# Kernel tuning notes

Measured on AMD Instinct MI355X. Metric: run time of the kernel, lower is better.

## Reference

```python
import jax, jax.numpy as jnp
import numpy as np

B, K, C, H, W = 32, 4, 256, 32, 32
MID = 32  # ceil((C//8)/8)*8
EPS = 1e-5


def setup_inputs() -> dict:
    key = jax.random.key(0)
    ks = jax.random.split(key, 8)
    scale1 = 1.0 / np.sqrt((K + 1) * C)
    scale2 = 1.0 / np.sqrt(MID)
    return {
        "y": jax.random.normal(ks[0], (B, C, H, W), jnp.float32),
        "x0": jax.random.normal(ks[1], (B, C, H, W), jnp.float32),
        "x1": jax.random.normal(ks[2], (B, C, H, W), jnp.float32),
        "x2": jax.random.normal(ks[3], (B, C, H, W), jnp.float32),
        "x3": jax.random.normal(ks[4], (B, C, H, W), jnp.float32),
        "conv1_w": jax.random.normal(ks[5], (MID, (K + 1) * C), jnp.float32) * scale1,
        "bn_gamma": jnp.ones((MID,), jnp.float32),
        "bn_beta": jnp.zeros((MID,), jnp.float32),
        "bn_mean": jnp.zeros((MID,), jnp.float32),
        "bn_var": jnp.ones((MID,), jnp.float32),
        "conv2_w": jax.random.normal(ks[6], ((K + 1) * C, MID), jnp.float32) * scale2,
        "conv2_b": jnp.zeros(((K + 1) * C,), jnp.float32),
    }


def reference(y, x0, x1, x2, x3, conv1_w, bn_gamma, bn_beta, bn_mean, bn_var, conv2_w, conv2_b):
    # Stack K branch feature maps: [B, K, C, H, W]
    xs = jnp.stack([x0, x1, x2, x3], axis=1)
    # Global-average-pooled gate features (1x1 spatial -> plain vectors)
    m_y = jnp.mean(y, axis=(2, 3))            # [B, C]
    m_x = jnp.mean(xs, axis=(3, 4))           # [B, K, C]
    feats = jnp.concatenate([m_y[:, None, :], m_x], axis=1).reshape(B, (K + 1) * C)
    # 1x1 conv -> BN (inference) -> ReLU -> 1x1 conv (all on 1x1 spatial = GEMM)
    h = feats @ conv1_w.T                      # [B, MID]
    h = (h - bn_mean) * (bn_gamma / jnp.sqrt(bn_var + EPS)) + bn_beta
    h = jax.nn.relu(h)
    w = (h @ conv2_w.T + conv2_b).reshape(B, K + 1, C)
    w1 = jax.nn.sigmoid(w[:, 0])               # [B, C] self gate
    w2 = jax.nn.softmax(w[:, 1:], axis=1)      # [B, K, C] branch gates (softmax over K)
    # Gated weighted sum of branches (GatedFunction.forward)
    z = jnp.einsum('bkc,bkchw->bchw', w2, xs)
    return y * w1[:, :, None, None] + z
```

## Files before the change

### kernel.cpp

```cpp
#include <hip/hip_runtime.h>
#include <math.h>

#define B 32
#define K 4
#define C 256
#define HW 1024
#define NT 5
#define MID 32
#define FEAT 1280
#define EPS 1e-5f

__global__ __launch_bounds__(256) void mean_kernel(
    const float* __restrict__ y,
    const float* __restrict__ x0, const float* __restrict__ x1,
    const float* __restrict__ x2, const float* __restrict__ x3,
    float* __restrict__ feats)
{
    const int wave = (blockIdx.x << 2) + (threadIdx.x >> 6);
    const int lane = threadIdx.x & 63;
    const int t    = wave >> 11;
    const int rem  = wave & 2047;
    const int b    = rem >> 6;
    const int g    = rem & 63;
    const float* src = (t == 0) ? y : (t == 1) ? x0 : (t == 2) ? x1
                                    : (t == 3) ? x2 : x3;
    const float4* p = (const float4*)(src + ((size_t)(b * C) + g * 4) * HW);

    float4 v[4][4];
#pragma unroll
    for (int s = 0; s < 4; ++s)
#pragma unroll
        for (int j = 0; j < 4; ++j)
            v[s][j] = p[s * 256 + j * 64 + lane];

    float s0 = 0.f, s1 = 0.f, s2 = 0.f, s3 = 0.f;
#pragma unroll
    for (int j = 0; j < 4; ++j) {
        s0 += v[0][j].x + v[0][j].y + v[0][j].z + v[0][j].w;
        s1 += v[1][j].x + v[1][j].y + v[1][j].z + v[1][j].w;
        s2 += v[2][j].x + v[2][j].y + v[2][j].z + v[2][j].w;
        s3 += v[3][j].x + v[3][j].y + v[3][j].z + v[3][j].w;
    }
#pragma unroll
    for (int m = 32; m >= 1; m >>= 1) {
        s0 += __shfl_xor(s0, m);
        s1 += __shfl_xor(s1, m);
        s2 += __shfl_xor(s2, m);
        s3 += __shfl_xor(s3, m);
    }
    if (lane == 0) {
        float4 r = make_float4(s0, s1, s2, s3);
        r.x *= (1.0f / 1024.0f); r.y *= (1.0f / 1024.0f);
        r.z *= (1.0f / 1024.0f); r.w *= (1.0f / 1024.0f);
        *((float4*)&feats[b * FEAT + t * C + g * 4]) = r;
    }
}

__global__ __launch_bounds__(512) void gate_kernel(
    const float* __restrict__ feats,
    const float* __restrict__ conv1_w,
    const float* __restrict__ bn_gamma, const float* __restrict__ bn_beta,
    const float* __restrict__ bn_mean,  const float* __restrict__ bn_var,
    const float* __restrict__ conv2_w,
    const float* __restrict__ conv2_b,
    float* __restrict__ gates)
{
    __shared__ __align__(16) float feats_s[FEAT];
    __shared__ float h_s[MID];

    const int b    = blockIdx.x;
    const int tid  = threadIdx.x;
    const int wave = tid >> 6;
    const int lane = tid & 63;

    for (int i = tid; i < FEAT; i += 512) feats_s[i] = feats[b * FEAT + i];
    __syncthreads();

    const float4* fs = (const float4*)feats_s;
    float4 wv[4][5];
#pragma unroll
    for (int r = 0; r < 4; ++r) {
        const float4* wp = (const float4*)(conv1_w + (wave * 4 + r) * FEAT);
#pragma unroll
        for (int k = 0; k < 5; ++k) wv[r][k] = wp[lane + 64 * k];
    }
    float a0 = 0.f, a1 = 0.f, a2 = 0.f, a3 = 0.f;
#pragma unroll
    for (int k = 0; k < 5; ++k) {
        float4 f = fs[lane + 64 * k];
        a0 += wv[0][k].x * f.x + wv[0][k].y * f.y + wv[0][k].z * f.z + wv[0][k].w * f.w;
        a1 += wv[1][k].x * f.x + wv[1][k].y * f.y + wv[1][k].z * f.z + wv[1][k].w * f.w;
        a2 += wv[2][k].x * f.x + wv[2][k].y * f.y + wv[2][k].z * f.z + wv[2][k].w * f.w;
        a3 += wv[3][k].x * f.x + wv[3][k].y * f.y + wv[3][k].z * f.z + wv[3][k].w * f.w;
    }
#pragma unroll
    for (int m = 32; m >= 1; m >>= 1) {
        a0 += __shfl_xor(a0, m);
        a1 += __shfl_xor(a1, m);
        a2 += __shfl_xor(a2, m);
        a3 += __shfl_xor(a3, m);
    }
    if (lane == 0) {
        float acc[4] = {a0, a1, a2, a3};
#pragma unroll
        for (int r = 0; r < 4; ++r) {
            const int m = wave * 4 + r;
            float inv = rsqrtf(bn_var[m] + EPS);
            float hv  = (acc[r] - bn_mean[m]) * (bn_gamma[m] * inv) + bn_beta[m];
            h_s[m] = fmaxf(hv, 0.f);
        }
    }
    __syncthreads();

    if (tid < 256) {
        float wvout[5];
#pragma unroll
        for (int r = 0; r < 5; ++r) {
            const int j = r * 256 + tid;
            const float4* w2 = (const float4*)(conv2_w + j * MID);
            float a = conv2_b[j];
#pragma unroll
            for (int i = 0; i < 8; ++i) {
                float4 q = w2[i];
                a += q.x * h_s[i * 4]     + q.y * h_s[i * 4 + 1]
                   + q.z * h_s[i * 4 + 2] + q.w * h_s[i * 4 + 3];
            }
            wvout[r] = a;
        }
        const float w1 = 1.f / (1.f + expf(-wvout[0]));
        const float mx = fmaxf(fmaxf(wvout[1], wvout[2]), fmaxf(wvout[3], wvout[4]));
        const float e1 = expf(wvout[1] - mx), e2 = expf(wvout[2] - mx);
        const float e3 = expf(wvout[3] - mx), e4 = expf(wvout[4] - mx);
        const float inv = 1.f / (e1 + e2 + e3 + e4);
        gates[b * FEAT +        tid] = w1;
        gates[b * FEAT +  256 + tid] = e1 * inv;
        gates[b * FEAT +  512 + tid] = e2 * inv;
        gates[b * FEAT +  768 + tid] = e3 * inv;
        gates[b * FEAT + 1024 + tid] = e4 * inv;
    }
}

__global__ __launch_bounds__(256) void out_kernel(
    const float* __restrict__ y,
    const float* __restrict__ x0, const float* __restrict__ x1,
    const float* __restrict__ x2, const float* __restrict__ x3,
    const float* __restrict__ gates,
    float* __restrict__ out)
{
    const int half  = threadIdx.x >> 7;
    const int idx   = threadIdx.x & 127;
    const int slice = blockIdx.x * 2 + half;
    const int b     = slice >> 8;
    const int c     = slice & 255;

    const float g0 = gates[b * FEAT +        c];
    const float g1 = gates[b * FEAT +  256 + c];
    const float g2 = gates[b * FEAT +  512 + c];
    const float g3 = gates[b * FEAT +  768 + c];
    const float g4 = gates[b * FEAT + 1024 + c];

    const size_t base = (size_t)slice * HW;
    const float4* py = (const float4*)(y  + base);
    const float4* p0 = (const float4*)(x0 + base);
    const float4* p1 = (const float4*)(x1 + base);
    const float4* p2 = (const float4*)(x2 + base);
    const float4* p3 = (const float4*)(x3 + base);

    float4 ya = py[idx], yb = py[idx + 128];
    float4 aa = p0[idx], ab = p0[idx + 128];
    float4 ba = p1[idx], bb = p1[idx + 128];
    float4 ca = p2[idx], cb = p2[idx + 128];
    float4 da = p3[idx], db = p3[idx + 128];

    float4 r0, r1;
    r0.x = ya.x * g0 + aa.x * g1 + ba.x * g2 + ca.x * g3 + da.x * g4;
    r0.y = ya.y * g0 + aa.y * g1 + ba.y * g2 + ca.y * g3 + da.y * g4;
    r0.z = ya.z * g0 + aa.z * g1 + ba.z * g2 + ca.z * g3 + da.z * g4;
    r0.w = ya.w * g0 + aa.w * g1 + ba.w * g2 + ca.w * g3 + da.w * g4;
    r1.x = yb.x * g0 + ab.x * g1 + bb.x * g2 + cb.x * g3 + db.x * g4;
    r1.y = yb.y * g0 + ab.y * g1 + bb.y * g2 + cb.y * g3 + db.y * g4;
    r1.z = yb.z * g0 + ab.z * g1 + bb.z * g2 + cb.z * g3 + db.z * g4;
    r1.w = yb.w * g0 + ab.w * g1 + bb.w * g2 + cb.w * g3 + db.w * g4;

    float4* po = (float4*)(out + base);
    po[idx]       = r0;
    po[idx + 128] = r1;
}

extern "C" void kernel_launch(void* const* d_in, const int* in_sizes, int n_in,
                              void* d_out, int out_size, void* d_ws, size_t ws_size,
                              hipStream_t stream) {
    const float* y        = (const float*)d_in[0];
    const float* x0       = (const float*)d_in[1];
    const float* x1       = (const float*)d_in[2];
    const float* x2       = (const float*)d_in[3];
    const float* x3       = (const float*)d_in[4];
    const float* conv1_w  = (const float*)d_in[5];
    const float* bn_gamma = (const float*)d_in[6];
    const float* bn_beta  = (const float*)d_in[7];
    const float* bn_mean  = (const float*)d_in[8];
    const float* bn_var   = (const float*)d_in[9];
    const float* conv2_w  = (const float*)d_in[10];
    const float* conv2_b  = (const float*)d_in[11];

    float* feats = (float*)d_ws;
    float* gates = feats + B * FEAT;
    float* out   = (float*)d_out;

    mean_kernel<<<(NT * B * C / 4) / 4, 256, 0, stream>>>(y, x0, x1, x2, x3, feats);
    gate_kernel<<<B, 512, 0, stream>>>(feats, conv1_w, bn_gamma, bn_beta,
                                       bn_mean, bn_var, conv2_w, conv2_b, gates);
    out_kernel<<<B * C / 2, 256, 0, stream>>>(y, x0, x1, x2, x3, gates, out);
}
```

Baseline: 233.9 us.

## Use one wave per channel in mean kernel and grid-stride the output kernel

The mean kernel now assigns one wave per (tensor, batch, channel) plane instead of four channels per wave, which gives four times as many smaller waves, fewer registers and a scalar store per plane. The output kernel becomes a persistent grid-stride loop over float4 elements with 2048 blocks, re-reading the five gate values for each element. The aim is better occupancy and latency hiding in these bandwidth-bound passes. The cost is more per-element gate loads and index math, and less memory-level parallelism per thread in the mean kernel.

```diff
diff --git a/kernel.cpp b/kernel.cpp
--- a/kernel.cpp
+++ b/kernel.cpp
@@ -10,50 +10,37 @@
 #define FEAT 1280
 #define EPS 1e-5f
 
+#define OUT_F4   (B * C * HW / 4)
+#define K3_BLKS  2048
+#define K3_THR   256
+#define K3_TOT   (K3_BLKS * K3_THR)
+
 __global__ __launch_bounds__(256) void mean_kernel(
     const float* __restrict__ y,
     const float* __restrict__ x0, const float* __restrict__ x1,
     const float* __restrict__ x2, const float* __restrict__ x3,
     float* __restrict__ feats)
 {
-    const int wave = (blockIdx.x << 2) + (threadIdx.x >> 6);
-    const int lane = threadIdx.x & 63;
-    const int t    = wave >> 11;
-    const int rem  = wave & 2047;
-    const int b    = rem >> 6;
-    const int g    = rem & 63;
+    int wave = (blockIdx.x << 2) + (threadIdx.x >> 6);
+    int lane = threadIdx.x & 63;
+    int t   = wave / (B * C);
+    int rem = wave - t * (B * C);
+    int b   = rem >> 8;
+    int c   = rem & 255;
     const float* src = (t == 0) ? y : (t == 1) ? x0 : (t == 2) ? x1
                                     : (t == 3) ? x2 : x3;
-    const float4* p = (const float4*)(src + ((size_t)(b * C) + g * 4) * HW);
-
-    float4 v[4][4];
+    const float4* p = (const float4*)(src + (size_t)(b * C + c) * HW);
+    float4 v0 = p[lane];
+    float4 v1 = p[lane + 64];
+    float4 v2 = p[lane + 128];
+    float4 v3 = p[lane + 192];
+    float s = v0.x + v0.y + v0.z + v0.w
+            + v1.x + v1.y + v1.z + v1.w
+            + v2.x + v2.y + v2.z + v2.w
+            + v3.x + v3.y + v3.z + v3.w;
 #pragma unroll
-    for (int s = 0; s < 4; ++s)
-#pragma unroll
-        for (int j = 0; j < 4; ++j)
-            v[s][j] = p[s * 256 + j * 64 + lane];
-
-    float s0 = 0.f, s1 = 0.f, s2 = 0.f, s3 = 0.f;
-#pragma unroll
-    for (int j = 0; j < 4; ++j) {
-        s0 += v[0][j].x + v[0][j].y + v[0][j].z + v[0][j].w;
-        s1 += v[1][j].x + v[1][j].y + v[1][j].z + v[1][j].w;
-        s2 += v[2][j].x + v[2][j].y + v[2][j].z + v[2][j].w;
-        s3 += v[3][j].x + v[3][j].y + v[3][j].z + v[3][j].w;
-    }
-#pragma unroll
-    for (int m = 32; m >= 1; m >>= 1) {
-        s0 += __shfl_xor(s0, m);
-        s1 += __shfl_xor(s1, m);
-        s2 += __shfl_xor(s2, m);
-        s3 += __shfl_xor(s3, m);
-    }
-    if (lane == 0) {
-        float4 r = make_float4(s0, s1, s2, s3);
-        r.x *= (1.0f / 1024.0f); r.y *= (1.0f / 1024.0f);
-        r.z *= (1.0f / 1024.0f); r.w *= (1.0f / 1024.0f);
-        *((float4*)&feats[b * FEAT + t * C + g * 4]) = r;
-    }
+    for (int m = 32; m >= 1; m >>= 1) s += __shfl_xor(s, m);
+    if (lane == 0) feats[b * FEAT + t * C + c] = s * (1.0f / 1024.0f);
 }
 
 __global__ __launch_bounds__(512) void gate_kernel(
@@ -140,51 +127,36 @@
     }
 }
 
-__global__ __launch_bounds__(256) void out_kernel(
+__global__ __launch_bounds__(K3_THR) void out_kernel(
     const float* __restrict__ y,
     const float* __restrict__ x0, const float* __restrict__ x1,
     const float* __restrict__ x2, const float* __restrict__ x3,
     const float* __restrict__ gates,
     float* __restrict__ out)
 {
-    const int half  = threadIdx.x >> 7;
-    const int idx   = threadIdx.x & 127;
-    const int slice = blockIdx.x * 2 + half;
-    const int b     = slice >> 8;
-    const int c     = slice & 255;
-
-    const float g0 = gates[b * FEAT +        c];
-    const float g1 = gates[b * FEAT +  256 + c];
-    const float g2 = gates[b * FEAT +  512 + c];
-    const float g3 = gates[b * FEAT +  768 + c];
-    const float g4 = gates[b * FEAT + 1024 + c];
-
-    const size_t base = (size_t)slice * HW;
-    const float4* py = (const float4*)(y  + base);
-    const float4* p0 = (const float4*)(x0 + base);
-    const float4* p1 = (const float4*)(x1 + base);
-    const float4* p2 = (const float4*)(x2 + base);
-    const float4* p3 = (const float4*)(x3 + base);
-
-    float4 ya = py[idx], yb = py[idx + 128];
-    float4 aa = p0[idx], ab = p0[idx + 128];
-    float4 ba = p1[idx], bb = p1[idx + 128];
-    float4 ca = p2[idx], cb = p2[idx + 128];
-    float4 da = p3[idx], db = p3[idx + 128];
-
-    float4 r0, r1;
-    r0.x = ya.x * g0 + aa.x * g1 + ba.x * g2 + ca.x * g3 + da.x * g4;
-    r0.y = ya.y * g0 + aa.y * g1 + ba.y * g2 + ca.y * g3 + da.y * g4;
-    r0.z = ya.z * g0 + aa.z * g1 + ba.z * g2 + ca.z * g3 + da.z * g4;
-    r0.w = ya.w * g0 + aa.w * g1 + ba.w * g2 + ca.w * g3 + da.w * g4;
-    r1.x = yb.x * g0 + ab.x * g1 + bb.x * g2 + cb.x * g3 + db.x * g4;
-    r1.y = yb.y * g0 + ab.y * g1 + bb.y * g2 + cb.y * g3 + db.y * g4;
-    r1.z = yb.z * g0 + ab.z * g1 + bb.z * g2 + cb.z * g3 + db.z * g4;
-    r1.w = yb.w * g0 + ab.w * g1 + bb.w * g2 + cb.w * g3 + db.w * g4;
-
-    float4* po = (float4*)(out + base);
-    po[idx]       = r0;
-    po[idx + 128] = r1;
+    const int gtid = blockIdx.x * K3_THR + threadIdx.x;
+    const float4* py = (const float4*)y;
+    const float4* p0 = (const float4*)x0;
+    const float4* p1 = (const float4*)x1;
+    const float4* p2 = (const float4*)x2;
+    const float4* p3 = (const float4*)x3;
+    float4* po = (float4*)out;
+#pragma unroll 2
+    for (int f = gtid; f < OUT_F4; f += K3_TOT) {
+        const int slice = f >> 8;
+        const int b = slice >> 8;
+        const int c = slice & 255;
+        const float* gb = gates + b * FEAT + c;
+        const float g0 = gb[0],   g1 = gb[256], g2 = gb[512];
+        const float g3 = gb[768], g4 = gb[1024];
+        float4 vy = py[f], v0 = p0[f], v1 = p1[f], v2 = p2[f], v3 = p3[f];
+        float4 r;
+        r.x = vy.x * g0 + v0.x * g1 + v1.x * g2 + v2.x * g3 + v3.x * g4;
+        r.y = vy.y * g0 + v0.y * g1 + v1.y * g2 + v2.y * g3 + v3.y * g4;
+        r.z = vy.z * g0 + v0.z * g1 + v1.z * g2 + v2.z * g3 + v3.z * g4;
+        r.w = vy.w * g0 + v0.w * g1 + v1.w * g2 + v2.w * g3 + v3.w * g4;
+        po[f] = r;
+    }
 }
 
 extern "C" void kernel_launch(void* const* d_in, const int* in_sizes, int n_in,
@@ -207,8 +179,8 @@
     float* gates = feats + B * FEAT;
     float* out   = (float*)d_out;
 
-    mean_kernel<<<(NT * B * C / 4) / 4, 256, 0, stream>>>(y, x0, x1, x2, x3, feats);
+    mean_kernel<<<(NT * B * C) / 4, 256, 0, stream>>>(y, x0, x1, x2, x3, feats);
     gate_kernel<<<B, 512, 0, stream>>>(feats, conv1_w, bn_gamma, bn_beta,
                                        bn_mean, bn_var, conv2_w, conv2_b, gates);
-    out_kernel<<<B * C / 2, 256, 0, stream>>>(y, x0, x1, x2, x3, gates, out);
+    out_kernel<<<K3_BLKS, K3_THR, 0, stream>>>(y, x0, x1, x2, x3, gates, out);
 }
```

Result: no change. 234.1 us (+0.1%).
